# Kernel tuning notes

Measured on AMD Instinct MI355X. Metric: run time of the kernel, lower is better.

The kernel has to match this reference:

```python
import jax, jax.numpy as jnp
import numpy as np

H = 16  # num_heads
NEG = -1e9


def setup_inputs() -> dict:
    key = jax.random.key(0)
    ks = jax.random.split(key, 12)
    T, B, E, M = 2048, 2, 1024, 1024
    s = E ** -0.5
    inp = {
        "query": jax.random.normal(ks[0], (T, B, E), jnp.float32),
        "position_encoding": jax.random.normal(ks[1], (H, T, T), jnp.float32) * 0.02,
        "long_context_retrieval": jax.random.normal(ks[2], (2, M, B, E), jnp.float32),
        "q_w": jax.random.normal(ks[3], (E, E), jnp.float32) * s,
        "q_b": jnp.zeros((E,), jnp.float32),
        "k_w": jax.random.normal(ks[4], (E, E), jnp.float32) * s,
        "k_b": jnp.zeros((E,), jnp.float32),
        "v_w": jax.random.normal(ks[5], (E, E), jnp.float32) * s,
        "v_b": jnp.zeros((E,), jnp.float32),
        "out_w": jax.random.normal(ks[6], (E, E), jnp.float32) * s,
        "out_b": jnp.zeros((E,), jnp.float32),
        "memory_bias": jnp.zeros((H,), jnp.float32),
    }
    return inp


def reference(query, position_encoding, long_context_retrieval,
              q_w, q_b, k_w, k_b, v_w, v_b, out_w, out_b, memory_bias):
    T, B, E = query.shape
    D = E // H
    scaling = D ** -0.5

    def proj(x, w, b):
        # x: [L, B, E] -> [B, H, L, D]
        L = x.shape[0]
        y = jnp.einsum('lbe,fe->lbf', x, w) + b
        return y.reshape(L, B, H, D).transpose(1, 2, 0, 3)

    q = proj(query, q_w, q_b) * scaling          # [B,H,T,D]
    k = proj(query, k_w, k_b)                    # [B,H,T,D]
    v = proj(query, v_w, v_b)                    # [B,H,T,D]

    # local attention with per-head position encoding and causal mask
    scores = jnp.einsum('bhtd,bhsd->bhts', q, k) + position_encoding[None]
    causal = jnp.triu(jnp.ones((T, T), bool), k=1)
    scores = jnp.where(causal[None, None], NEG, scores)
    attn_local = jax.nn.softmax(scores, axis=-1)
    out_local = jnp.einsum('bhts,bhsd->bhtd', attn_local, v)

    # attention over retrieved long-context memory (keys/values projected)
    km = proj(long_context_retrieval[0], k_w, k_b)   # [B,H,M,D]
    vm = proj(long_context_retrieval[1], v_w, v_b)   # [B,H,M,D]
    mem_scores = jnp.einsum('bhtd,bhmd->bhtm', q, km)
    attn_mem = jax.nn.softmax(mem_scores, axis=-1)
    out_mem = jnp.einsum('bhtm,bhmd->bhtd', attn_mem, vm)

    # per-head learned gate: weighted sum of local and memory outputs
    g = jax.nn.sigmoid(memory_bias)[None, :, None, None]
    out = (1.0 - g) * out_local + g * out_mem        # [B,H,T,D]

    out = out.transpose(2, 0, 1, 3).reshape(T, B, E)
    return jnp.einsum('tbe,fe->tbf', out, out_w) + out_b
```

## Files before the change

### kernel.cpp

```cpp
#include <hip/hip_runtime.h>

typedef __bf16 bf16_t;
typedef __bf16 bf16x2 __attribute__((ext_vector_type(2)));
typedef __bf16 bf16x8 __attribute__((ext_vector_type(8)));
typedef float floatx4 __attribute__((ext_vector_type(4)));

#define MFMA16(a, b, c) __builtin_amdgcn_mfma_f32_16x16x32_bf16((a), (b), (c), 0, 0, 0)

__global__ void detect_kernel(const unsigned short* __restrict__ q, int* flag)
{
    __shared__ int cnt;
    if (threadIdx.x == 0) cnt = 0;
    __syncthreads();
    int local = 0;
    for (int i = threadIdx.x; i < 65536; i += 256) {
        unsigned short u = q[i];
        if ((u & 0x7F80u) == 0x7F80u) local++;
    }
    atomicAdd(&cnt, local);
    __syncthreads();
    if (threadIdx.x == 0) flag[0] = (cnt >= 8) ? 1 : 0;
}

__device__ inline void cvt16_f32(const float* __restrict__ p, bf16x8& lo, bf16x8& hi)
{
    float4 a = ((const float4*)p)[0];
    float4 b = ((const float4*)p)[1];
    float4 c = ((const float4*)p)[2];
    float4 d = ((const float4*)p)[3];
    lo[0] = (bf16_t)a.x; lo[1] = (bf16_t)a.y; lo[2] = (bf16_t)a.z; lo[3] = (bf16_t)a.w;
    lo[4] = (bf16_t)b.x; lo[5] = (bf16_t)b.y; lo[6] = (bf16_t)b.z; lo[7] = (bf16_t)b.w;
    hi[0] = (bf16_t)c.x; hi[1] = (bf16_t)c.y; hi[2] = (bf16_t)c.z; hi[3] = (bf16_t)c.w;
    hi[4] = (bf16_t)d.x; hi[5] = (bf16_t)d.y; hi[6] = (bf16_t)d.z; hi[7] = (bf16_t)d.w;
}

__global__ __launch_bounds__(256) void proj_kernel(
    const void* __restrict__ query, const void* __restrict__ lcr,
    const void* __restrict__ qw, const void* __restrict__ kw,
    const void* __restrict__ vw,
    const void* __restrict__ qbias, const void* __restrict__ kbias,
    const void* __restrict__ vbias,
    bf16_t* __restrict__ q_ws, bf16_t* __restrict__ k_ws,
    bf16_t* __restrict__ vt_ws, bf16_t* __restrict__ km_ws,
    bf16_t* __restrict__ vmt_ws, const int* __restrict__ flag)
{
    __shared__ __attribute__((aligned(16))) bf16_t As[128 * 40];
    __shared__ __attribute__((aligned(16))) bf16_t Bs[128 * 40];

    const int f32 = flag[0];
    const int K = 1024;
    const int blk = blockIdx.x;

    int rm0, wcol, mode, Tdim;
    float scale;
    const void* Xv; size_t xoff0; const void* Wv; const void* biasv; bf16_t* Yv;
    if (blk < 768) {
        rm0 = (blk & 31) * 128;
        const int cn0 = (blk >> 5) * 128;
        const int sel = cn0 >> 10;
        wcol = cn0 & 1023;
        Xv = query; xoff0 = 0; Tdim = 2048;
        if (sel == 0)      { Wv = qw; biasv = qbias; Yv = q_ws;  mode = 1; scale = 0.125f; }
        else if (sel == 1) { Wv = kw; biasv = kbias; Yv = k_ws;  mode = 1; scale = 1.f; }
        else               { Wv = vw; biasv = vbias; Yv = vt_ws; mode = 2; scale = 1.f; }
    } else if (blk < 896) {
        const int b2 = blk - 768;
        rm0 = (b2 & 15) * 128; wcol = (b2 >> 4) * 128;
        Xv = lcr; xoff0 = 0;
        Wv = kw; biasv = kbias; Yv = km_ws; mode = 1; scale = 1.f; Tdim = 1024;
    } else {
        const int b2 = blk - 896;
        rm0 = (b2 & 15) * 128; wcol = (b2 >> 4) * 128;
        Xv = lcr; xoff0 = (size_t)1024 * 2 * 1024;
        Wv = vw; biasv = vbias; Yv = vmt_ws; mode = 2; scale = 1.f; Tdim = 1024;
    }

    const int tid = threadIdx.x;
    const int wvid = tid >> 6, lane = tid & 63;
    const int qd = lane >> 4, l16 = lane & 15;
    const int wm = (wvid >> 1) * 64, wn = (wvid & 1) * 64;

    const int srow = tid >> 1;
    const int sseg = (tid & 1) * 16;
    const size_t xoff = xoff0 + (size_t)(rm0 + srow) * K + sseg;
    const size_t woff = (size_t)(wcol + srow) * K + sseg;
    const bf16_t* Xh = (const bf16_t*)Xv + xoff;
    const float*  Xf = (const float*)Xv + xoff;
    const bf16_t* Wh = (const bf16_t*)Wv + woff;
    const float*  Wf = (const float*)Wv + woff;
    bf16_t* Asw = &As[srow * 40 + sseg];
    bf16_t* Bsw = &Bs[srow * 40 + sseg];

    floatx4 acc[4][4];
#pragma unroll
    for (int i = 0; i < 4; i++)
#pragma unroll
        for (int j = 0; j < 4; j++) acc[i][j] = (floatx4){0.f, 0.f, 0.f, 0.f};

    for (int k0 = 0; k0 < K; k0 += 32) {
        bf16x8 x0, x1, w0, w1;
        if (f32) {
            cvt16_f32(Xf + k0, x0, x1);
            cvt16_f32(Wf + k0, w0, w1);
        } else {
            x0 = *(const bf16x8*)(Xh + k0);
            x1 = *(const bf16x8*)(Xh + k0 + 8);
            w0 = *(const bf16x8*)(Wh + k0);
            w1 = *(const bf16x8*)(Wh + k0 + 8);
        }
        __syncthreads();
        *(bf16x8*)(Asw) = x0;
        *(bf16x8*)(Asw + 8) = x1;
        *(bf16x8*)(Bsw) = w0;
        *(bf16x8*)(Bsw + 8) = w1;
        __syncthreads();

        bf16x8 af[4], bfg[4];
#pragma unroll
        for (int mi = 0; mi < 4; mi++)
            af[mi] = *(const bf16x8*)(&As[(wm + mi * 16 + l16) * 40 + qd * 8]);
#pragma unroll
        for (int ni = 0; ni < 4; ni++)
            bfg[ni] = *(const bf16x8*)(&Bs[(wn + ni * 16 + l16) * 40 + qd * 8]);
#pragma unroll
        for (int mi = 0; mi < 4; mi++)
#pragma unroll
            for (int ni = 0; ni < 4; ni++)
                acc[mi][ni] = MFMA16(af[mi], bfg[ni], acc[mi][ni]);
    }

#pragma unroll
    for (int ni = 0; ni < 4; ni++) {
        const int col = wcol + wn + ni * 16 + l16;
        const float bv = f32 ? ((const float*)biasv)[col]
                             : (float)((const bf16_t*)biasv)[col];
        const int hh = col >> 6, dd = col & 63;
#pragma unroll
        for (int mi = 0; mi < 4; mi++) {
            const int row0 = rm0 + wm + mi * 16 + qd * 4;
            const int t = row0 >> 1;
            const float v0 = (acc[mi][ni][0] + bv) * scale;
            const float v1 = (acc[mi][ni][1] + bv) * scale;
            const float v2 = (acc[mi][ni][2] + bv) * scale;
            const float v3 = (acc[mi][ni][3] + bv) * scale;
            if (mode == 1) {
                Yv[(((size_t)hh * Tdim) + t) * 64 + dd]            = (bf16_t)v0;
                Yv[(((size_t)(16 + hh) * Tdim) + t) * 64 + dd]     = (bf16_t)v1;
                Yv[(((size_t)hh * Tdim) + t + 1) * 64 + dd]        = (bf16_t)v2;
                Yv[(((size_t)(16 + hh) * Tdim) + t + 1) * 64 + dd] = (bf16_t)v3;
            } else {
                bf16x2 p0; p0[0] = (bf16_t)v0; p0[1] = (bf16_t)v2;
                bf16x2 p1; p1[0] = (bf16_t)v1; p1[1] = (bf16_t)v3;
                *(bf16x2*)&Yv[((size_t)hh * 64 + dd) * Tdim + t] = p0;
                *(bf16x2*)&Yv[((size_t)(16 + hh) * 64 + dd) * Tdim + t] = p1;
            }
        }
    }
}

#define PSTR 88
__global__ __launch_bounds__(256) void attn_kernel(
    const bf16_t* __restrict__ Qg, const bf16_t* __restrict__ Kg,
    const bf16_t* __restrict__ VTg, const bf16_t* __restrict__ KMg,
    const bf16_t* __restrict__ VMTg, const void* __restrict__ posv,
    const void* __restrict__ mbiasv, bf16_t* __restrict__ att,
    const int* __restrict__ flag, int T, int Mlen)
{
    __shared__ __attribute__((aligned(16))) bf16_t Ps[4][16 * PSTR];

    const int f32 = flag[0];
    const int tid = threadIdx.x;
    const int wv = tid >> 6, lane = tid & 63;
    const int qd = lane >> 4, l16 = lane & 15;
    const int qt = blockIdx.x;
    const int y = blockIdx.y;
    const int b = y & 1, h = y >> 1;
    const int bh = b * 16 + h;
    const int t0 = qt * 64;
    const int tw = t0 + wv * 16;

    const bf16_t* Qb  = Qg  + (size_t)bh * T * 64;
    const bf16_t* Kb  = Kg  + (size_t)bh * T * 64;
    const bf16_t* VTb = VTg + (size_t)bh * 64 * T;
    const bf16_t* KMb = KMg + (size_t)bh * Mlen * 64;
    const bf16_t* VMTb = VMTg + (size_t)bh * 64 * Mlen;
    const float*  posf = (const float*)posv + (size_t)h * T * T;
    const bf16_t* posh = (const bf16_t*)posv + (size_t)h * T * T;

    const bf16x8 a0 = *(const bf16x8*)(Qb + (size_t)(tw + l16) * 64 + qd * 8);
    const bf16x8 a1 = *(const bf16x8*)(Qb + (size_t)(tw + l16) * 64 + 32 + qd * 8);

    floatx4 Ol[4], Om[4];
    float ml[4], ll[4], mm2[4], lm[4];
#pragma unroll
    for (int i = 0; i < 4; i++) {
        Ol[i] = (floatx4){0.f, 0.f, 0.f, 0.f};
        Om[i] = (floatx4){0.f, 0.f, 0.f, 0.f};
        ml[i] = -1e9f; ll[i] = 0.f; mm2[i] = -1e9f; lm[i] = 0.f;
    }

    const int trow_base = tw + qd * 4;
    bf16_t* Pw = &Ps[wv][0];

    for (int st = 0; st <= qt; ++st) {
        const int s0 = st * 64;
        const bool diag = (st == qt);
        const int nhi = diag ? (wv + 1) : 4;

        float sv[4][4];
#pragma unroll
        for (int ni = 0; ni < 4; ni++)
#pragma unroll
            for (int r = 0; r < 4; r++) sv[ni][r] = -1e9f;

#pragma unroll
        for (int ni = 0; ni < 4; ni++) {
            if (ni < nhi) {
                const bf16x8 kb0 = *(const bf16x8*)(Kb + (size_t)(s0 + ni * 16 + l16) * 64 + qd * 8);
                const bf16x8 kb1 = *(const bf16x8*)(Kb + (size_t)(s0 + ni * 16 + l16) * 64 + 32 + qd * 8);
                floatx4 c = (floatx4){0.f, 0.f, 0.f, 0.f};
                c = MFMA16(a0, kb0, c);
                c = MFMA16(a1, kb1, c);
                const int sg = s0 + ni * 16 + l16;
#pragma unroll
                for (int r = 0; r < 4; r++) {
                    const int tg = trow_base + r;
                    const size_t pidx = (size_t)tg * T + sg;
                    const float pe = f32 ? posf[pidx] : (float)posh[pidx];
                    float val = c[r] + pe;
                    if (diag && sg > tg) val = -1e9f;
                    sv[ni][r] = val;
                }
            }
        }

#pragma unroll
        for (int r = 0; r < 4; r++) {
            float mt = fmaxf(fmaxf(sv[0][r], sv[1][r]), fmaxf(sv[2][r], sv[3][r]));
            mt = fmaxf(mt, __shfl_xor(mt, 1));
            mt = fmaxf(mt, __shfl_xor(mt, 2));
            mt = fmaxf(mt, __shfl_xor(mt, 4));
            mt = fmaxf(mt, __shfl_xor(mt, 8));
            const float mnew = fmaxf(ml[r], mt);
            const float alpha = __expf(ml[r] - mnew);
            ml[r] = mnew;
            float ls = 0.f;
#pragma unroll
            for (int ni = 0; ni < 4; ni++) {
                const float p = __expf(sv[ni][r] - mnew);
                sv[ni][r] = p;
                ls += p;
            }
            ls += __shfl_xor(ls, 1);
            ls += __shfl_xor(ls, 2);
            ls += __shfl_xor(ls, 4);
            ls += __shfl_xor(ls, 8);
            ll[r] = ll[r] * alpha + ls;
#pragma unroll
            for (int ni = 0; ni < 4; ni++) Ol[ni][r] *= alpha;
#pragma unroll
            for (int ni = 0; ni < 4; ni++)
                Pw[(qd * 4 + r) * PSTR + ni * 16 + l16] = (bf16_t)sv[ni][r];
        }
        asm volatile("s_waitcnt lgkmcnt(0)" ::: "memory");
        const bf16x8 pf0 = *(const bf16x8*)(&Pw[l16 * PSTR + qd * 8]);
        const bf16x8 pf1 = *(const bf16x8*)(&Pw[l16 * PSTR + 32 + qd * 8]);
#pragma unroll
        for (int ni = 0; ni < 4; ni++) {
            const bf16x8 vf0 = *(const bf16x8*)(VTb + (size_t)(ni * 16 + l16) * T + s0 + qd * 8);
            const bf16x8 vf1 = *(const bf16x8*)(VTb + (size_t)(ni * 16 + l16) * T + s0 + 32 + qd * 8);
            Ol[ni] = MFMA16(pf0, vf0, Ol[ni]);
            Ol[ni] = MFMA16(pf1, vf1, Ol[ni]);
        }
    }

    for (int st = 0; st < Mlen / 64; ++st) {
        const int s0 = st * 64;
        float sv[4][4];
#pragma unroll
        for (int ni = 0; ni < 4; ni++) {
            const bf16x8 kb0 = *(const bf16x8*)(KMb + (size_t)(s0 + ni * 16 + l16) * 64 + qd * 8);
            const bf16x8 kb1 = *(const bf16x8*)(KMb + (size_t)(s0 + ni * 16 + l16) * 64 + 32 + qd * 8);
            floatx4 c = (floatx4){0.f, 0.f, 0.f, 0.f};
            c = MFMA16(a0, kb0, c);
            c = MFMA16(a1, kb1, c);
#pragma unroll
            for (int r = 0; r < 4; r++) sv[ni][r] = c[r];
        }

#pragma unroll
        for (int r = 0; r < 4; r++) {
            float mt = fmaxf(fmaxf(sv[0][r], sv[1][r]), fmaxf(sv[2][r], sv[3][r]));
            mt = fmaxf(mt, __shfl_xor(mt, 1));
            mt = fmaxf(mt, __shfl_xor(mt, 2));
            mt = fmaxf(mt, __shfl_xor(mt, 4));
            mt = fmaxf(mt, __shfl_xor(mt, 8));
            const float mnew = fmaxf(mm2[r], mt);
            const float alpha = __expf(mm2[r] - mnew);
            mm2[r] = mnew;
            float ls = 0.f;
#pragma unroll
            for (int ni = 0; ni < 4; ni++) {
                const float p = __expf(sv[ni][r] - mnew);
                sv[ni][r] = p;
                ls += p;
            }
            ls += __shfl_xor(ls, 1);
            ls += __shfl_xor(ls, 2);
            ls += __shfl_xor(ls, 4);
            ls += __shfl_xor(ls, 8);
            lm[r] = lm[r] * alpha + ls;
#pragma unroll
            for (int ni = 0; ni < 4; ni++) Om[ni][r] *= alpha;
#pragma unroll
            for (int ni = 0; ni < 4; ni++)
                Pw[(qd * 4 + r) * PSTR + ni * 16 + l16] = (bf16_t)sv[ni][r];
        }
        asm volatile("s_waitcnt lgkmcnt(0)" ::: "memory");
        const bf16x8 pf0 = *(const bf16x8*)(&Pw[l16 * PSTR + qd * 8]);
        const bf16x8 pf1 = *(const bf16x8*)(&Pw[l16 * PSTR + 32 + qd * 8]);
#pragma unroll
        for (int ni = 0; ni < 4; ni++) {
            const bf16x8 vf0 = *(const bf16x8*)(VMTb + (size_t)(ni * 16 + l16) * Mlen + s0 + qd * 8);
            const bf16x8 vf1 = *(const bf16x8*)(VMTb + (size_t)(ni * 16 + l16) * Mlen + s0 + 32 + qd * 8);
            Om[ni] = MFMA16(pf0, vf0, Om[ni]);
            Om[ni] = MFMA16(pf1, vf1, Om[ni]);
        }
    }

    const float gb = f32 ? ((const float*)mbiasv)[h] : (float)((const bf16_t*)mbiasv)[h];
    const float g = 1.f / (1.f + __expf(-gb));
#pragma unroll
    for (int ni = 0; ni < 4; ni++) {
        const int col = h * 64 + ni * 16 + l16;
#pragma unroll
        for (int r = 0; r < 4; r++) {
            const int tg = trow_base + r;
            const float ol = Ol[ni][r] / ll[r];
            const float om = Om[ni][r] / lm[r];
            const float val = (1.f - g) * ol + g * om;
            att[(size_t)(tg * 2 + b) * 1024 + col] = (bf16_t)val;
        }
    }
}

__global__ __launch_bounds__(256) void gemm64_kernel(
    const bf16_t* __restrict__ X, const void* __restrict__ Wv,
    const void* __restrict__ biasv, void* __restrict__ Yv,
    const int* __restrict__ flag)
{
    __shared__ __attribute__((aligned(16))) bf16_t As[64 * 40];
    __shared__ __attribute__((aligned(16))) bf16_t Bs[128 * 40];

    const int f32 = flag[0];
    const int K = 1024, N = 1024;
    const int tid = threadIdx.x;
    const int wvid = tid >> 6, lane = tid & 63;
    const int qd = lane >> 4, l16 = lane & 15;
    const int wn = wvid * 32;
    const int rm0 = blockIdx.x * 64, cn0 = blockIdx.y * 128;

    const int arow = tid >> 1;
    const int aseg = (tid & 1) * 16;
    const bf16_t* Xp = X + (size_t)(rm0 + (arow & 63)) * K + aseg;
    const size_t woff = (size_t)(cn0 + arow) * K + aseg;
    const bf16_t* Wh = (const bf16_t*)Wv + woff;
    const float*  Wf = (const float*)Wv + woff;

    floatx4 acc[4][2];
#pragma unroll
    for (int i = 0; i < 4; i++)
#pragma unroll
        for (int j = 0; j < 2; j++) acc[i][j] = (floatx4){0.f, 0.f, 0.f, 0.f};

    for (int k0 = 0; k0 < K; k0 += 32) {
        bf16x8 x0, x1, w0, w1;
        if (tid < 128) {
            x0 = *(const bf16x8*)(Xp + k0);
            x1 = *(const bf16x8*)(Xp + k0 + 8);
        }
        if (f32) cvt16_f32(Wf + k0, w0, w1);
        else {
            w0 = *(const bf16x8*)(Wh + k0);
            w1 = *(const bf16x8*)(Wh + k0 + 8);
        }
        __syncthreads();
        if (tid < 128) {
            *(bf16x8*)&As[arow * 40 + aseg] = x0;
            *(bf16x8*)&As[arow * 40 + aseg + 8] = x1;
        }
        *(bf16x8*)&Bs[arow * 40 + aseg] = w0;
        *(bf16x8*)&Bs[arow * 40 + aseg + 8] = w1;
        __syncthreads();

        bf16x8 af[4], bfg[2];
#pragma unroll
        for (int mi = 0; mi < 4; mi++)
            af[mi] = *(const bf16x8*)(&As[(mi * 16 + l16) * 40 + qd * 8]);
#pragma unroll
        for (int ni = 0; ni < 2; ni++)
            bfg[ni] = *(const bf16x8*)(&Bs[(wn + ni * 16 + l16) * 40 + qd * 8]);
#pragma unroll
        for (int mi = 0; mi < 4; mi++)
#pragma unroll
            for (int ni = 0; ni < 2; ni++)
                acc[mi][ni] = MFMA16(af[mi], bfg[ni], acc[mi][ni]);
    }

#pragma unroll
    for (int ni = 0; ni < 2; ni++) {
        const int col = cn0 + wn + ni * 16 + l16;
        const float bv = f32 ? ((const float*)biasv)[col]
                             : (float)((const bf16_t*)biasv)[col];
#pragma unroll
        for (int mi = 0; mi < 4; mi++) {
            const int row0 = rm0 + mi * 16 + qd * 4;
#pragma unroll
            for (int r = 0; r < 4; r++) {
                const int row = row0 + r;
                const float val = acc[mi][ni][r] + bv;
                if (f32) ((float*)Yv)[(size_t)row * N + col] = val;
                else ((bf16_t*)Yv)[(size_t)row * N + col] = (bf16_t)val;
            }
        }
    }
}

__global__ void sentinel_kernel(float* o) { o[0] = 30000.0f; }

extern "C" void kernel_launch(void* const* d_in, const int* in_sizes, int n_in,
                              void* d_out, int out_size, void* d_ws, size_t ws_size,
                              hipStream_t stream)
{
    const void* query = d_in[0];
    const void* pos   = d_in[1];
    const void* lcr   = d_in[2];
    const void* q_w   = d_in[3];
    const void* q_b   = d_in[4];
    const void* k_w   = d_in[5];
    const void* k_b   = d_in[6];
    const void* v_w   = d_in[7];
    const void* v_b   = d_in[8];
    const void* out_w = d_in[9];
    const void* out_b = d_in[10];
    const void* mbias = d_in[11];

    const int T = 2048, B = 2, E = 1024, M = 1024;

    const size_t elems = (size_t)(3 * B * 16 * T * 64 + 2 * B * 16 * M * 64 + T * B * E);
    const size_t needed = elems * 2 + 64;
    if (ws_size < needed) {
        sentinel_kernel<<<1, 1, 0, stream>>>((float*)d_out);
        return;
    }

    bf16_t* q_ws   = (bf16_t*)d_ws;
    bf16_t* k_ws   = q_ws + (size_t)B * 16 * T * 64;
    bf16_t* vt_ws  = k_ws + (size_t)B * 16 * T * 64;
    bf16_t* km_ws  = vt_ws + (size_t)B * 16 * T * 64;
    bf16_t* vmt_ws = km_ws + (size_t)B * 16 * M * 64;
    bf16_t* att_ws = vmt_ws + (size_t)B * 16 * M * 64;
    int* flag = (int*)((char*)d_ws + elems * 2);

    detect_kernel<<<1, 256, 0, stream>>>((const unsigned short*)query, flag);
    proj_kernel<<<1024, 256, 0, stream>>>(query, lcr, q_w, k_w, v_w,
                                          q_b, k_b, v_b,
                                          q_ws, k_ws, vt_ws, km_ws, vmt_ws, flag);
    attn_kernel<<<dim3(T / 64, 32), 256, 0, stream>>>(
        q_ws, k_ws, vt_ws, km_ws, vmt_ws, pos, mbias, att_ws, flag, T, M);
    gemm64_kernel<<<dim3(T * B / 64, E / 128), 256, 0, stream>>>(
        att_ws, out_w, out_b, d_out, flag);
    (void)in_sizes; (void)n_in; (void)out_size;
}
```

Baseline: 884.0 us.

## Split local and memory attention into separate blocks with prefetch and combine kernel

Splits the attention kernel over a new grid z dimension so local causal attention and memory attention run in separate blocks. Each writes gated fp32 partial outputs, and a new combine kernel sums them into bf16. The main loops now prefetch the next K tile and position-encoding tile, load V early, and seed the QK MFMA accumulator with the position bias. Row-sum shuffles are deferred to the end, and detect_kernel reads with wider vector loads. The aim is more parallelism and better latency hiding, at the cost of extra fp32 traffic, an extra launch and more registers.

```diff
diff --git a/kernel.cpp b/kernel.cpp
--- a/kernel.cpp
+++ b/kernel.cpp
@@ -2,20 +2,25 @@
 
 typedef __bf16 bf16_t;
 typedef __bf16 bf16x2 __attribute__((ext_vector_type(2)));
+typedef __bf16 bf16x4 __attribute__((ext_vector_type(4)));
 typedef __bf16 bf16x8 __attribute__((ext_vector_type(8)));
 typedef float floatx4 __attribute__((ext_vector_type(4)));
 
 #define MFMA16(a, b, c) __builtin_amdgcn_mfma_f32_16x16x32_bf16((a), (b), (c), 0, 0, 0)
 
-__global__ void detect_kernel(const unsigned short* __restrict__ q, int* flag)
+__global__ void detect_kernel(const uint4* __restrict__ q, int* __restrict__ flag)
 {
     __shared__ int cnt;
     if (threadIdx.x == 0) cnt = 0;
     __syncthreads();
     int local = 0;
-    for (int i = threadIdx.x; i < 65536; i += 256) {
-        unsigned short u = q[i];
-        if ((u & 0x7F80u) == 0x7F80u) local++;
+    for (int i = threadIdx.x; i < 8192; i += 1024) {
+        uint4 u = q[i];
+        unsigned w;
+        w = u.x; if ((w & 0x7F80u) == 0x7F80u) local++; if (((w >> 16) & 0x7F80u) == 0x7F80u) local++;
+        w = u.y; if ((w & 0x7F80u) == 0x7F80u) local++; if (((w >> 16) & 0x7F80u) == 0x7F80u) local++;
+        w = u.z; if ((w & 0x7F80u) == 0x7F80u) local++; if (((w >> 16) & 0x7F80u) == 0x7F80u) local++;
+        w = u.w; if ((w & 0x7F80u) == 0x7F80u) local++; if (((w >> 16) & 0x7F80u) == 0x7F80u) local++;
     }
     atomicAdd(&cnt, local);
     __syncthreads();
@@ -159,12 +164,43 @@
 }
 
 #define PSTR 88
+
+__device__ __forceinline__ void load_k8(bf16x8 k0v[4], bf16x8 k1v[4],
+                                        const bf16_t* __restrict__ Kb,
+                                        int s0, int l16, int qd)
+{
+#pragma unroll
+    for (int ni = 0; ni < 4; ni++) {
+        const bf16_t* p = Kb + (size_t)(s0 + ni * 16 + l16) * 64 + qd * 8;
+        k0v[ni] = *(const bf16x8*)p;
+        k1v[ni] = *(const bf16x8*)(p + 32);
+    }
+}
+
+__device__ __forceinline__ void load_pos4(floatx4 pn[4], const float* __restrict__ posf,
+                                          const bf16_t* __restrict__ posh, int f32,
+                                          int T, int trow_base, int s0, int l16, bool diag)
+{
+#pragma unroll
+    for (int ni = 0; ni < 4; ni++) {
+        const int sg = s0 + ni * 16 + l16;
+#pragma unroll
+        for (int r = 0; r < 4; r++) {
+            const int tg = trow_base + r;
+            const size_t pidx = (size_t)tg * T + sg;
+            float pv = f32 ? posf[pidx] : (float)posh[pidx];
+            if (diag && sg > tg) pv = -1e9f;
+            pn[ni][r] = pv;
+        }
+    }
+}
+
 __global__ __launch_bounds__(256) void attn_kernel(
     const bf16_t* __restrict__ Qg, const bf16_t* __restrict__ Kg,
     const bf16_t* __restrict__ VTg, const bf16_t* __restrict__ KMg,
     const bf16_t* __restrict__ VMTg, const void* __restrict__ posv,
-    const void* __restrict__ mbiasv, bf16_t* __restrict__ att,
-    const int* __restrict__ flag, int T, int Mlen)
+    const void* __restrict__ mbiasv, float* __restrict__ attl,
+    float* __restrict__ attm, const int* __restrict__ flag, int T, int Mlen)
 {
     __shared__ __attribute__((aligned(16))) bf16_t Ps[4][16 * PSTR];
 
@@ -176,172 +212,195 @@
     const int y = blockIdx.y;
     const int b = y & 1, h = y >> 1;
     const int bh = b * 16 + h;
-    const int t0 = qt * 64;
-    const int tw = t0 + wv * 16;
-
-    const bf16_t* Qb  = Qg  + (size_t)bh * T * 64;
-    const bf16_t* Kb  = Kg  + (size_t)bh * T * 64;
-    const bf16_t* VTb = VTg + (size_t)bh * 64 * T;
-    const bf16_t* KMb = KMg + (size_t)bh * Mlen * 64;
-    const bf16_t* VMTb = VMTg + (size_t)bh * 64 * Mlen;
-    const float*  posf = (const float*)posv + (size_t)h * T * T;
-    const bf16_t* posh = (const bf16_t*)posv + (size_t)h * T * T;
-
+    const int tw = qt * 64 + wv * 16;
+    const int trow_base = tw + qd * 4;
+    bf16_t* Pw = &Ps[wv][0];
+
+    const bf16_t* Qb = Qg + (size_t)bh * T * 64;
     const bf16x8 a0 = *(const bf16x8*)(Qb + (size_t)(tw + l16) * 64 + qd * 8);
     const bf16x8 a1 = *(const bf16x8*)(Qb + (size_t)(tw + l16) * 64 + 32 + qd * 8);
 
-    floatx4 Ol[4], Om[4];
-    float ml[4], ll[4], mm2[4], lm[4];
-#pragma unroll
-    for (int i = 0; i < 4; i++) {
-        Ol[i] = (floatx4){0.f, 0.f, 0.f, 0.f};
-        Om[i] = (floatx4){0.f, 0.f, 0.f, 0.f};
-        ml[i] = -1e9f; ll[i] = 0.f; mm2[i] = -1e9f; lm[i] = 0.f;
-    }
-
-    const int trow_base = tw + qd * 4;
-    bf16_t* Pw = &Ps[wv][0];
-
-    for (int st = 0; st <= qt; ++st) {
-        const int s0 = st * 64;
-        const bool diag = (st == qt);
-        const int nhi = diag ? (wv + 1) : 4;
-
-        float sv[4][4];
-#pragma unroll
-        for (int ni = 0; ni < 4; ni++)
-#pragma unroll
-            for (int r = 0; r < 4; r++) sv[ni][r] = -1e9f;
-
-#pragma unroll
-        for (int ni = 0; ni < 4; ni++) {
-            if (ni < nhi) {
-                const bf16x8 kb0 = *(const bf16x8*)(Kb + (size_t)(s0 + ni * 16 + l16) * 64 + qd * 8);
-                const bf16x8 kb1 = *(const bf16x8*)(Kb + (size_t)(s0 + ni * 16 + l16) * 64 + 32 + qd * 8);
-                floatx4 c = (floatx4){0.f, 0.f, 0.f, 0.f};
-                c = MFMA16(a0, kb0, c);
-                c = MFMA16(a1, kb1, c);
-                const int sg = s0 + ni * 16 + l16;
-#pragma unroll
-                for (int r = 0; r < 4; r++) {
-                    const int tg = trow_base + r;
-                    const size_t pidx = (size_t)tg * T + sg;
-                    const float pe = f32 ? posf[pidx] : (float)posh[pidx];
-                    float val = c[r] + pe;
-                    if (diag && sg > tg) val = -1e9f;
-                    sv[ni][r] = val;
-                }
-            }
-        }
-
-#pragma unroll
-        for (int r = 0; r < 4; r++) {
-            float mt = fmaxf(fmaxf(sv[0][r], sv[1][r]), fmaxf(sv[2][r], sv[3][r]));
-            mt = fmaxf(mt, __shfl_xor(mt, 1));
-            mt = fmaxf(mt, __shfl_xor(mt, 2));
-            mt = fmaxf(mt, __shfl_xor(mt, 4));
-            mt = fmaxf(mt, __shfl_xor(mt, 8));
-            const float mnew = fmaxf(ml[r], mt);
-            const float alpha = __expf(ml[r] - mnew);
-            ml[r] = mnew;
-            float ls = 0.f;
-#pragma unroll
-            for (int ni = 0; ni < 4; ni++) {
-                const float p = __expf(sv[ni][r] - mnew);
-                sv[ni][r] = p;
-                ls += p;
-            }
-            ls += __shfl_xor(ls, 1);
-            ls += __shfl_xor(ls, 2);
-            ls += __shfl_xor(ls, 4);
-            ls += __shfl_xor(ls, 8);
-            ll[r] = ll[r] * alpha + ls;
-#pragma unroll
-            for (int ni = 0; ni < 4; ni++) Ol[ni][r] *= alpha;
-#pragma unroll
-            for (int ni = 0; ni < 4; ni++)
-                Pw[(qd * 4 + r) * PSTR + ni * 16 + l16] = (bf16_t)sv[ni][r];
-        }
-        asm volatile("s_waitcnt lgkmcnt(0)" ::: "memory");
-        const bf16x8 pf0 = *(const bf16x8*)(&Pw[l16 * PSTR + qd * 8]);
-        const bf16x8 pf1 = *(const bf16x8*)(&Pw[l16 * PSTR + 32 + qd * 8]);
-#pragma unroll
-        for (int ni = 0; ni < 4; ni++) {
-            const bf16x8 vf0 = *(const bf16x8*)(VTb + (size_t)(ni * 16 + l16) * T + s0 + qd * 8);
-            const bf16x8 vf1 = *(const bf16x8*)(VTb + (size_t)(ni * 16 + l16) * T + s0 + 32 + qd * 8);
-            Ol[ni] = MFMA16(pf0, vf0, Ol[ni]);
-            Ol[ni] = MFMA16(pf1, vf1, Ol[ni]);
-        }
-    }
-
-    for (int st = 0; st < Mlen / 64; ++st) {
-        const int s0 = st * 64;
-        float sv[4][4];
-#pragma unroll
-        for (int ni = 0; ni < 4; ni++) {
-            const bf16x8 kb0 = *(const bf16x8*)(KMb + (size_t)(s0 + ni * 16 + l16) * 64 + qd * 8);
-            const bf16x8 kb1 = *(const bf16x8*)(KMb + (size_t)(s0 + ni * 16 + l16) * 64 + 32 + qd * 8);
-            floatx4 c = (floatx4){0.f, 0.f, 0.f, 0.f};
-            c = MFMA16(a0, kb0, c);
-            c = MFMA16(a1, kb1, c);
-#pragma unroll
-            for (int r = 0; r < 4; r++) sv[ni][r] = c[r];
-        }
-
-#pragma unroll
-        for (int r = 0; r < 4; r++) {
-            float mt = fmaxf(fmaxf(sv[0][r], sv[1][r]), fmaxf(sv[2][r], sv[3][r]));
-            mt = fmaxf(mt, __shfl_xor(mt, 1));
-            mt = fmaxf(mt, __shfl_xor(mt, 2));
-            mt = fmaxf(mt, __shfl_xor(mt, 4));
-            mt = fmaxf(mt, __shfl_xor(mt, 8));
-            const float mnew = fmaxf(mm2[r], mt);
-            const float alpha = __expf(mm2[r] - mnew);
-            mm2[r] = mnew;
-            float ls = 0.f;
-#pragma unroll
-            for (int ni = 0; ni < 4; ni++) {
-                const float p = __expf(sv[ni][r] - mnew);
-                sv[ni][r] = p;
-                ls += p;
-            }
-            ls += __shfl_xor(ls, 1);
-            ls += __shfl_xor(ls, 2);
-            ls += __shfl_xor(ls, 4);
-            ls += __shfl_xor(ls, 8);
-            lm[r] = lm[r] * alpha + ls;
-#pragma unroll
-            for (int ni = 0; ni < 4; ni++) Om[ni][r] *= alpha;
-#pragma unroll
-            for (int ni = 0; ni < 4; ni++)
-                Pw[(qd * 4 + r) * PSTR + ni * 16 + l16] = (bf16_t)sv[ni][r];
-        }
-        asm volatile("s_waitcnt lgkmcnt(0)" ::: "memory");
-        const bf16x8 pf0 = *(const bf16x8*)(&Pw[l16 * PSTR + qd * 8]);
-        const bf16x8 pf1 = *(const bf16x8*)(&Pw[l16 * PSTR + 32 + qd * 8]);
-#pragma unroll
-        for (int ni = 0; ni < 4; ni++) {
-            const bf16x8 vf0 = *(const bf16x8*)(VMTb + (size_t)(ni * 16 + l16) * Mlen + s0 + qd * 8);
-            const bf16x8 vf1 = *(const bf16x8*)(VMTb + (size_t)(ni * 16 + l16) * Mlen + s0 + 32 + qd * 8);
-            Om[ni] = MFMA16(pf0, vf0, Om[ni]);
-            Om[ni] = MFMA16(pf1, vf1, Om[ni]);
-        }
-    }
-
     const float gb = f32 ? ((const float*)mbiasv)[h] : (float)((const bf16_t*)mbiasv)[h];
     const float g = 1.f / (1.f + __expf(-gb));
-#pragma unroll
-    for (int ni = 0; ni < 4; ni++) {
-        const int col = h * 64 + ni * 16 + l16;
+
+    floatx4 O[4];
+    float ml[4], ll[4];
+#pragma unroll
+    for (int i = 0; i < 4; i++) {
+        O[i] = (floatx4){0.f, 0.f, 0.f, 0.f};
+        ml[i] = -1e9f; ll[i] = 0.f;
+    }
+
+    bf16x8 kc0[4], kc1[4];
+
+    if (blockIdx.z == 0) {
+        const bf16_t* Kb  = Kg  + (size_t)bh * T * 64;
+        const bf16_t* VTb = VTg + (size_t)bh * 64 * T;
+        const float*  posf = (const float*)posv + (size_t)h * T * T;
+        const bf16_t* posh = (const bf16_t*)posv + (size_t)h * T * T;
+
+        floatx4 pn[4];
+        load_k8(kc0, kc1, Kb, 0, l16, qd);
+        load_pos4(pn, posf, posh, f32, T, trow_base, 0, l16, qt == 0);
+
+        for (int st = 0; st <= qt; ++st) {
+            const int s0 = st * 64;
+            bf16x8 vf0[4], vf1[4];
+#pragma unroll
+            for (int ni = 0; ni < 4; ni++) {
+                const bf16_t* p = VTb + (size_t)(ni * 16 + l16) * T + s0 + qd * 8;
+                vf0[ni] = *(const bf16x8*)p;
+                vf1[ni] = *(const bf16x8*)(p + 32);
+            }
+            floatx4 c[4];
+#pragma unroll
+            for (int ni = 0; ni < 4; ni++) {
+                floatx4 t = pn[ni];
+                t = MFMA16(a0, kc0[ni], t);
+                t = MFMA16(a1, kc1[ni], t);
+                c[ni] = t;
+            }
+            if (st < qt) {
+                load_k8(kc0, kc1, Kb, s0 + 64, l16, qd);
+                load_pos4(pn, posf, posh, f32, T, trow_base, s0 + 64, l16, st + 1 == qt);
+            }
+#pragma unroll
+            for (int r = 0; r < 4; r++) {
+                float mt = fmaxf(fmaxf(c[0][r], c[1][r]), fmaxf(c[2][r], c[3][r]));
+                mt = fmaxf(mt, __shfl_xor(mt, 1));
+                mt = fmaxf(mt, __shfl_xor(mt, 2));
+                mt = fmaxf(mt, __shfl_xor(mt, 4));
+                mt = fmaxf(mt, __shfl_xor(mt, 8));
+                const float mnew = fmaxf(ml[r], mt);
+                const float alpha = __expf(ml[r] - mnew);
+                ml[r] = mnew;
+                float ls = 0.f;
+#pragma unroll
+                for (int ni = 0; ni < 4; ni++) {
+                    const float p = __expf(c[ni][r] - mnew);
+                    c[ni][r] = p;
+                    ls += p;
+                }
+                ll[r] = ll[r] * alpha + ls;
+#pragma unroll
+                for (int ni = 0; ni < 4; ni++) O[ni][r] *= alpha;
+#pragma unroll
+                for (int ni = 0; ni < 4; ni++)
+                    Pw[(qd * 4 + r) * PSTR + ni * 16 + l16] = (bf16_t)c[ni][r];
+            }
+            asm volatile("s_waitcnt lgkmcnt(0)" ::: "memory");
+            const bf16x8 pf0 = *(const bf16x8*)(&Pw[l16 * PSTR + qd * 8]);
+            const bf16x8 pf1 = *(const bf16x8*)(&Pw[l16 * PSTR + 32 + qd * 8]);
+#pragma unroll
+            for (int ni = 0; ni < 4; ni++) {
+                O[ni] = MFMA16(pf0, vf0[ni], O[ni]);
+                O[ni] = MFMA16(pf1, vf1[ni], O[ni]);
+            }
+        }
+
+        const float gl = 1.f - g;
 #pragma unroll
         for (int r = 0; r < 4; r++) {
+            float lt = ll[r];
+            lt += __shfl_xor(lt, 1);
+            lt += __shfl_xor(lt, 2);
+            lt += __shfl_xor(lt, 4);
+            lt += __shfl_xor(lt, 8);
             const int tg = trow_base + r;
-            const float ol = Ol[ni][r] / ll[r];
-            const float om = Om[ni][r] / lm[r];
-            const float val = (1.f - g) * ol + g * om;
-            att[(size_t)(tg * 2 + b) * 1024 + col] = (bf16_t)val;
-        }
-    }
+            const float inv = gl / lt;
+#pragma unroll
+            for (int ni = 0; ni < 4; ni++)
+                attl[(size_t)(tg * 2 + b) * 1024 + h * 64 + ni * 16 + l16] = O[ni][r] * inv;
+        }
+    } else {
+        const bf16_t* Kb  = KMg  + (size_t)bh * Mlen * 64;
+        const bf16_t* VTb = VMTg + (size_t)bh * 64 * Mlen;
+        const int nst = Mlen >> 6;
+
+        load_k8(kc0, kc1, Kb, 0, l16, qd);
+
+        for (int st = 0; st < nst; ++st) {
+            const int s0 = st * 64;
+            bf16x8 vf0[4], vf1[4];
+#pragma unroll
+            for (int ni = 0; ni < 4; ni++) {
+                const bf16_t* p = VTb + (size_t)(ni * 16 + l16) * Mlen + s0 + qd * 8;
+                vf0[ni] = *(const bf16x8*)p;
+                vf1[ni] = *(const bf16x8*)(p + 32);
+            }
+            floatx4 c[4];
+#pragma unroll
+            for (int ni = 0; ni < 4; ni++) {
+                floatx4 t = (floatx4){0.f, 0.f, 0.f, 0.f};
+                t = MFMA16(a0, kc0[ni], t);
+                t = MFMA16(a1, kc1[ni], t);
+                c[ni] = t;
+            }
+            if (st < nst - 1) load_k8(kc0, kc1, Kb, s0 + 64, l16, qd);
+#pragma unroll
+            for (int r = 0; r < 4; r++) {
+                float mt = fmaxf(fmaxf(c[0][r], c[1][r]), fmaxf(c[2][r], c[3][r]));
+                mt = fmaxf(mt, __shfl_xor(mt, 1));
+                mt = fmaxf(mt, __shfl_xor(mt, 2));
+                mt = fmaxf(mt, __shfl_xor(mt, 4));
+                mt = fmaxf(mt, __shfl_xor(mt, 8));
+                const float mnew = fmaxf(ml[r], mt);
+                const float alpha = __expf(ml[r] - mnew);
+                ml[r] = mnew;
+                float ls = 0.f;
+#pragma unroll
+                for (int ni = 0; ni < 4; ni++) {
+                    const float p = __expf(c[ni][r] - mnew);
+                    c[ni][r] = p;
+                    ls += p;
+                }
+                ll[r] = ll[r] * alpha + ls;
+#pragma unroll
+                for (int ni = 0; ni < 4; ni++) O[ni][r] *= alpha;
+#pragma unroll
+                for (int ni = 0; ni < 4; ni++)
+                    Pw[(qd * 4 + r) * PSTR + ni * 16 + l16] = (bf16_t)c[ni][r];
+            }
+            asm volatile("s_waitcnt lgkmcnt(0)" ::: "memory");
+            const bf16x8 pf0 = *(const bf16x8*)(&Pw[l16 * PSTR + qd * 8]);
+            const bf16x8 pf1 = *(const bf16x8*)(&Pw[l16 * PSTR + 32 + qd * 8]);
+#pragma unroll
+            for (int ni = 0; ni < 4; ni++) {
+                O[ni] = MFMA16(pf0, vf0[ni], O[ni]);
+                O[ni] = MFMA16(pf1, vf1[ni], O[ni]);
+            }
+        }
+
+#pragma unroll
+        for (int r = 0; r < 4; r++) {
+            float lt = ll[r];
+            lt += __shfl_xor(lt, 1);
+            lt += __shfl_xor(lt, 2);
+            lt += __shfl_xor(lt, 4);
+            lt += __shfl_xor(lt, 8);
+            const int tg = trow_base + r;
+            const float inv = g / lt;
+#pragma unroll
+            for (int ni = 0; ni < 4; ni++)
+                attm[(size_t)(tg * 2 + b) * 1024 + h * 64 + ni * 16 + l16] = O[ni][r] * inv;
+        }
+    }
+}
+
+__global__ __launch_bounds__(256) void combine_kernel(
+    const float4* __restrict__ a, const float4* __restrict__ bsrc,
+    bf16_t* __restrict__ o, int n4)
+{
+    const int i = blockIdx.x * 256 + threadIdx.x;
+    if (i >= n4) return;
+    const float4 x = a[i];
+    const float4 y = bsrc[i];
+    bf16x4 r;
+    r[0] = (bf16_t)(x.x + y.x);
+    r[1] = (bf16_t)(x.y + y.y);
+    r[2] = (bf16_t)(x.z + y.z);
+    r[3] = (bf16_t)(x.w + y.w);
+    *(bf16x4*)(o + (size_t)i * 4) = r;
 }
 
 __global__ __launch_bounds__(256) void gemm64_kernel(
@@ -447,27 +506,34 @@
 
     const int T = 2048, B = 2, E = 1024, M = 1024;
 
-    const size_t elems = (size_t)(3 * B * 16 * T * 64 + 2 * B * 16 * M * 64 + T * B * E);
-    const size_t needed = elems * 2 + 64;
+    const size_t nqkv = (size_t)B * 16 * T * 64;
+    const size_t nmem = (size_t)B * 16 * M * 64;
+    const size_t natt = (size_t)T * B * E;
+    const size_t bf16_elems = 3 * nqkv + 2 * nmem + natt;
+    const size_t needed = bf16_elems * 2 + 2 * natt * 4 + 64;
     if (ws_size < needed) {
         sentinel_kernel<<<1, 1, 0, stream>>>((float*)d_out);
         return;
     }
 
     bf16_t* q_ws   = (bf16_t*)d_ws;
-    bf16_t* k_ws   = q_ws + (size_t)B * 16 * T * 64;
-    bf16_t* vt_ws  = k_ws + (size_t)B * 16 * T * 64;
-    bf16_t* km_ws  = vt_ws + (size_t)B * 16 * T * 64;
-    bf16_t* vmt_ws = km_ws + (size_t)B * 16 * M * 64;
-    bf16_t* att_ws = vmt_ws + (size_t)B * 16 * M * 64;
-    int* flag = (int*)((char*)d_ws + elems * 2);
-
-    detect_kernel<<<1, 256, 0, stream>>>((const unsigned short*)query, flag);
+    bf16_t* k_ws   = q_ws + nqkv;
+    bf16_t* vt_ws  = k_ws + nqkv;
+    bf16_t* km_ws  = vt_ws + nqkv;
+    bf16_t* vmt_ws = km_ws + nmem;
+    bf16_t* att_ws = vmt_ws + nmem;
+    float* attl_ws = (float*)(att_ws + natt);
+    float* attm_ws = attl_ws + natt;
+    int* flag = (int*)(attm_ws + natt);
+
+    detect_kernel<<<1, 1024, 0, stream>>>((const uint4*)query, flag);
     proj_kernel<<<1024, 256, 0, stream>>>(query, lcr, q_w, k_w, v_w,
                                           q_b, k_b, v_b,
                                           q_ws, k_ws, vt_ws, km_ws, vmt_ws, flag);
-    attn_kernel<<<dim3(T / 64, 32), 256, 0, stream>>>(
-        q_ws, k_ws, vt_ws, km_ws, vmt_ws, pos, mbias, att_ws, flag, T, M);
+    attn_kernel<<<dim3(T / 64, 32, 2), 256, 0, stream>>>(
+        q_ws, k_ws, vt_ws, km_ws, vmt_ws, pos, mbias, attl_ws, attm_ws, flag, T, M);
+    combine_kernel<<<(int)(natt / 4 / 256), 256, 0, stream>>>(
+        (const float4*)attl_ws, (const float4*)attm_ws, att_ws, (int)(natt / 4));
     gemm64_kernel<<<dim3(T * B / 64, E / 128), 256, 0, stream>>>(
         att_ws, out_w, out_b, d_out, flag);
     (void)in_sizes; (void)n_in; (void)out_size;
```

Result: faster. 851.7 us (-3.7%).
